# Performance work log

Hardware: AMD Instinct MI355X
Metric: run time of the kernel (lower is better)

Reference implementation:

```python
import jax, jax.numpy as jnp
import numpy as np

W = 32  # voxel grid resolution, codebook size = W**3 = 32768


def _grid_points(w=W):
    # meshgrid of integer voxel indices, shape (3, w, w, w), then map to cell
    # centers in [-1, 1]: ((idx + 0.5) * 2 / w - 1), flattened to (w^3, 3).
    idx = np.stack(np.meshgrid(np.arange(w), np.arange(w), np.arange(w), indexing='ij'))
    pts = (idx + 0.5) * 2.0 / w - 1.0
    return jnp.asarray(pts.reshape(3, -1).T, dtype=jnp.float32)  # (32768, 3)


def setup_inputs() -> dict:
    key = jax.random.key(0)
    B, N = 4, 1024
    # points uniform in [-1, 1]^3
    x = jax.random.uniform(key, (B, N, 3), dtype=jnp.float32) * 2.0 - 1.0
    return {"x": x, "grid_points": _grid_points()}


def reference(x, grid_points):
    B, N, _ = x.shape
    K = grid_points.shape[0]  # 32768
    flat_x = x.reshape(B * N, 3)
    dists = (jnp.sum(flat_x ** 2, axis=1, keepdims=True)
             + jnp.sum(grid_points ** 2, axis=1)
             - 2.0 * flat_x @ grid_points.T)
    enc = jnp.argmin(dists, axis=1).reshape(B, N)
    enc = jnp.sort(enc, axis=1)  # (B, N) int
    # scatter ones into the occupied voxels (duplicates just re-set to 1)
    voxel = jnp.zeros((B, K), dtype=jnp.float32)
    voxel = voxel.at[jnp.arange(B)[:, None], enc].set(1.0)
    voxel = voxel.reshape(B, 1, W, W, W)
    voxel = (voxel - 0.5) / 0.5 * 0.8  # map {0,1} -> {-0.8, 0.8}
    return enc, voxel
```

## Files before the change

### kernel.cpp

```cpp
#include <hip/hip_runtime.h>


#define VW 32
#define VK (VW*VW*VW)
#define NPTS 1024
#define NB 4

__device__ __forceinline__ int cmpex_shfl(int v, int jj, int k, int t) {
    int pv = __shfl_xor(v, jj);
    bool keepmin = (((t & jj) == 0) == ((t & k) == 0));
    return keepmin ? min(v, pv) : max(v, pv);
}

__global__ __launch_bounds__(NPTS) void pq_kernel(const float* __restrict__ x,
                                                  float* __restrict__ out) {
    const int b = blockIdx.x;
    const int t = threadIdx.x;

    float* enc_out = out;
    float* vox = out + NB * NPTS + (size_t)b * VK;

    __shared__ int sb[2][NPTS];

    const float* p = x + (size_t)(b * NPTS + t) * 3;
    float px = p[0], py = p[1], pz = p[2];
    int i = min(max((int)floorf((px + 1.0f) * 16.0f), 0), VW - 1);
    int j = min(max((int)floorf((py + 1.0f) * 16.0f), 0), VW - 1);
    int l = min(max((int)floorf((pz + 1.0f) * 16.0f), 0), VW - 1);
    const int enc = i * (VW * VW) + j * VW + l;
    int v = enc;

    const float4 neg = make_float4(-0.8f, -0.8f, -0.8f, -0.8f);
    float4* v4 = (float4*)vox;
    #pragma unroll
    for (int r = 0; r < VK / 4 / NPTS; ++r)
        v4[r * NPTS + t] = neg;

    #pragma unroll
    for (int k = 2; k <= 64; k <<= 1)
        #pragma unroll
        for (int jj = k >> 1; jj > 0; jj >>= 1)
            v = cmpex_shfl(v, jj, k, t);

    int cur = 0;
    sb[0][t] = v;
    __syncthreads();
    vox[enc] = 0.8f;

    #pragma unroll
    for (int k = 128; k <= NPTS; k <<= 1) {
        for (int jj = k >> 1; jj >= 64; jj >>= 1) {
            int pv = sb[cur][t ^ jj];
            bool keepmin = (((t & jj) == 0) == ((t & k) == 0));
            v = keepmin ? min(v, pv) : max(v, pv);
            sb[cur ^ 1][t] = v;
            __syncthreads();
            cur ^= 1;
        }
        #pragma unroll
        for (int jj = 32; jj > 0; jj >>= 1)
            v = cmpex_shfl(v, jj, k, t);
        if (k < NPTS) {
            sb[cur ^ 1][t] = v;
            __syncthreads();
            cur ^= 1;
        }
    }

    enc_out[b * NPTS + t] = (float)v;
}

extern "C" void kernel_launch(void* const* d_in, const int* in_sizes, int n_in,
                              void* d_out, int out_size, void* d_ws, size_t ws_size,
                              hipStream_t stream) {
    const float* x = (const float*)d_in[0];
    float* out = (float*)d_out;

    pq_kernel<<<NB, NPTS, 0, stream>>>(x, out);
}
```

Before: 12.08 us.

## Build occupancy bitmap in LDS and write voxel grid in one pass

Each block now sets bits in a shared-memory occupancy bitmap with atomicOr, then writes every voxel float4 once with the final ±0.8 value. This removes the fill-then-scatter pattern, with its second scattered global write and the ordering it needs. It also swaps __syncthreads for a custom barrier that waits only on LDS counters, which avoids draining outstanding global stores at each sort step. The custom barrier depends on the compiler not reordering around the inline asm, and it adds two barriers plus LDS atomics up front.

```diff
diff --git a/kernel.cpp b/kernel.cpp
--- a/kernel.cpp
+++ b/kernel.cpp
@@ -5,6 +5,9 @@
 #define VK (VW*VW*VW)
 #define NPTS 1024
 #define NB 4
+#define NWORDS (VK/32)
+
+#define BARRIER_LDS() asm volatile("s_waitcnt lgkmcnt(0)\n\ts_barrier" ::: "memory")
 
 __device__ __forceinline__ int cmpex_shfl(int v, int jj, int k, int t) {
     int pv = __shfl_xor(v, jj);
@@ -20,21 +23,34 @@
     float* enc_out = out;
     float* vox = out + NB * NPTS + (size_t)b * VK;
 
+    __shared__ unsigned bm[NWORDS];
     __shared__ int sb[2][NPTS];
+
+    bm[t] = 0u;
 
     const float* p = x + (size_t)(b * NPTS + t) * 3;
     float px = p[0], py = p[1], pz = p[2];
     int i = min(max((int)floorf((px + 1.0f) * 16.0f), 0), VW - 1);
     int j = min(max((int)floorf((py + 1.0f) * 16.0f), 0), VW - 1);
     int l = min(max((int)floorf((pz + 1.0f) * 16.0f), 0), VW - 1);
-    const int enc = i * (VW * VW) + j * VW + l;
-    int v = enc;
+    int v = i * (VW * VW) + j * VW + l;
 
-    const float4 neg = make_float4(-0.8f, -0.8f, -0.8f, -0.8f);
+    BARRIER_LDS();
+    atomicOr(&bm[v >> 5], 1u << (v & 31));
+    BARRIER_LDS();
+
     float4* v4 = (float4*)vox;
     #pragma unroll
-    for (int r = 0; r < VK / 4 / NPTS; ++r)
-        v4[r * NPTS + t] = neg;
+    for (int g = 0; g < 8; ++g) {
+        int m = g * NPTS + t;
+        unsigned nib = bm[m >> 3] >> ((m & 7) * 4);
+        float4 f;
+        f.x = (nib & 1u) ? 0.8f : -0.8f;
+        f.y = (nib & 2u) ? 0.8f : -0.8f;
+        f.z = (nib & 4u) ? 0.8f : -0.8f;
+        f.w = (nib & 8u) ? 0.8f : -0.8f;
+        v4[m] = f;
+    }
 
     #pragma unroll
     for (int k = 2; k <= 64; k <<= 1)
@@ -44,8 +60,7 @@
 
     int cur = 0;
     sb[0][t] = v;
-    __syncthreads();
-    vox[enc] = 0.8f;
+    BARRIER_LDS();
 
     #pragma unroll
     for (int k = 128; k <= NPTS; k <<= 1) {
@@ -54,7 +69,7 @@
             bool keepmin = (((t & jj) == 0) == ((t & k) == 0));
             v = keepmin ? min(v, pv) : max(v, pv);
             sb[cur ^ 1][t] = v;
-            __syncthreads();
+            BARRIER_LDS();
             cur ^= 1;
         }
         #pragma unroll
@@ -62,7 +77,7 @@
             v = cmpex_shfl(v, jj, k, t);
         if (k < NPTS) {
             sb[cur ^ 1][t] = v;
-            __syncthreads();
+            BARRIER_LDS();
             cur ^= 1;
         }
     }
```

Result: faster. 10.78 us (-10.8%).
